# Performance work log

Hardware: AMD Instinct MI355X
Metric: run time of the kernel (lower is better)

## Reference

```python
import jax, jax.numpy as jnp
import numpy as np
import math

NH, NKV, HD = 8, 1, 128
SOFTCAP = 30.0
ROPE_BASE = 500000.0


def _rope_tables(T, hd, base):
    half = hd // 2
    inv_freq = 1.0 / (base ** (np.arange(half, dtype=np.float32) / half))
    t = np.arange(T, dtype=np.float32)
    ang = np.outer(t, inv_freq)  # [T, half]
    return jnp.asarray(np.cos(ang)), jnp.asarray(np.sin(ang))


def apply_rope(x, cos, sin):
    # x: [B, T, H, hd]; cos/sin: [T, hd//2]
    half = x.shape[-1] // 2
    x1, x2 = x[..., :half], x[..., half:]
    T = x.shape[1]
    c = cos[:T][None, :, None, :]
    s = sin[:T][None, :, None, :]
    return jnp.concatenate([x1 * c - x2 * s, x1 * s + x2 * c], axis=-1)


def setup_inputs() -> dict:
    key = jax.random.key(0)
    ks = jax.random.split(key, 5)
    B, T, D = 4, 2048, 1024
    KD = NKV * HD
    x = jax.random.normal(ks[0], (B, T, D), dtype=jnp.float32)
    Wq = jax.random.normal(ks[1], (D, D), dtype=jnp.float32) * (D ** -0.5)
    Wk = jax.random.normal(ks[2], (KD, D), dtype=jnp.float32) * (D ** -0.5)
    Wv = jax.random.normal(ks[3], (KD, D), dtype=jnp.float32) * (D ** -0.5)
    Wo = jax.random.normal(ks[4], (D, D), dtype=jnp.float32) * (D ** -0.5)
    qk_gain = jnp.full((NH,), 1.5, dtype=jnp.float32)  # qk_gain_init
    cos, sin = _rope_tables(T, HD, ROPE_BASE)
    return {"x": x, "Wq": Wq, "Wk": Wk, "Wv": Wv, "Wo": Wo,
            "qk_gain": qk_gain, "cos": cos, "sin": sin}


def reference(x, Wq, Wk, Wv, Wo, qk_gain, cos, sin):
    B, T, D = x.shape
    # projections (QuantLinear with qat disabled == plain linear, no bias)
    q = (x @ Wq.T).reshape(B, T, NH, HD)
    k = (x @ Wk.T).reshape(B, T, NKV, HD)
    v = (x @ Wv.T).reshape(B, T, NKV, HD)
    q = apply_rope(q, cos, sin)
    k = apply_rope(k, cos, sin)
    # learned per-head QK gain applied to queries
    q = q * qk_gain[None, None, :, 1 - 1][..., None] if False else q * qk_gain[None, None, :, None]
    # GQA: broadcast the single kv head across NH query heads
    scale = 1.0 / math.sqrt(HD)
    scores = jnp.einsum('bqhd,bkgd->bhqk', q, k) * scale  # g==NKV==1 broadcast
    # logit softcap before masking/softmax
    scores = SOFTCAP * jnp.tanh(scores / SOFTCAP)
    causal = jnp.tril(jnp.ones((T, T), dtype=bool))
    scores = jnp.where(causal[None, None], scores, -jnp.inf)
    attn = jax.nn.softmax(scores, axis=-1)  # [B, NH, T, T]
    out = jnp.einsum('bhqk,bkgd->bqhd', attn, v).reshape(B, T, NH * HD)
    return out @ Wo.T
```

## Files before the change

### kernel.cpp

```cpp
#include <hip/hip_runtime.h>
#include <hip/hip_bf16.h>

#define B_ 4
#define T_ 2048
#define D_ 1024
#define NH_ 8
#define HD_ 128

typedef short short8 __attribute__((ext_vector_type(8)));
typedef float floatx4 __attribute__((ext_vector_type(4)));
typedef float floatx16 __attribute__((ext_vector_type(16)));

#if __has_builtin(__builtin_amdgcn_exp2f)
#define EXP2F __builtin_amdgcn_exp2f
#else
#define EXP2F exp2f
#endif
#if __has_builtin(__builtin_amdgcn_rcpf)
#define RCPF __builtin_amdgcn_rcpf
#else
__device__ __forceinline__ float RCPF(float x) { return 1.f / x; }
#endif

#if __has_builtin(__builtin_amdgcn_global_load_lds)
#define G2L(gp, lp)                                                        \
  __builtin_amdgcn_global_load_lds(                                        \
      (const __attribute__((address_space(1))) unsigned int*)(gp),         \
      (__attribute__((address_space(3))) unsigned int*)(lp), 16, 0, 0)
#else
#define G2L(gp, lp) (*(uint4*)(lp) = *(const uint4*)(gp))
#endif

__device__ __forceinline__ unsigned short f2b(float f) {
  union { float fl; unsigned int i; } v; v.fl = f;
  unsigned int r = v.i + 0x7fffu + ((v.i >> 16) & 1u);
  return (unsigned short)(r >> 16);
}
__device__ __forceinline__ unsigned int pack_bf16(float a, float b) {
  unsigned int ua = __float_as_uint(a) + 0x8000u;
  unsigned int ub = __float_as_uint(b) + 0x8000u;
  return (ua >> 16) | (ub & 0xffff0000u);
}
__device__ __forceinline__ float blo(unsigned int u) { return __uint_as_float(u << 16); }
__device__ __forceinline__ float bhi(unsigned int u) { return __uint_as_float(u & 0xffff0000u); }

__global__ __launch_bounds__(256) void cvt_kernel(
    const float* __restrict__ x,  const float* __restrict__ wq,
    const float* __restrict__ wk, const float* __restrict__ wv,
    const float* __restrict__ wo, unsigned short* __restrict__ dst)
{
  size_t i = ((size_t)blockIdx.x * 256 + threadIdx.x) * 8;
  const float* src; size_t off;
  if      (i <  8388608u) { src = x;  off = i; }
  else if (i <  9437184u) { src = wq; off = i - 8388608u; }
  else if (i <  9568256u) { src = wk; off = i - 9437184u; }
  else if (i <  9699328u) { src = wv; off = i - 9568256u; }
  else                    { src = wo; off = i - 9699328u; }
  float4 a = *(const float4*)(src + off);
  float4 b = *(const float4*)(src + off + 4);
  uint4 o;
  o.x = pack_bf16(a.x, a.y); o.y = pack_bf16(a.z, a.w);
  o.z = pack_bf16(b.x, b.y); o.w = pack_bf16(b.z, b.w);
  *(uint4*)(dst + i) = o;
}

template <bool C_F32>
__device__ __forceinline__ void gemm_body_1024(
    const unsigned short* __restrict__ Arow0,
    const unsigned short* __restrict__ Btile,
    void* __restrict__ Cb, int ldC)
{
  __shared__ unsigned short As[128 * 32];
  __shared__ unsigned short Bs[128 * 32];
  const int tid = threadIdx.x;
  const int lane = tid & 63;
  const int w = tid >> 6;
  const int wr = w >> 1, wc = w & 1;
  const int l15 = lane & 15, quad = lane >> 4;

  const unsigned short* a_src = Arow0 + (size_t)(tid >> 2) * 1024 + (tid & 3) * 8;
  const unsigned short* b_src = Btile + (size_t)(tid >> 2) * 1024 + (tid & 3) * 8;
  unsigned short* a_dst = &As[(tid >> 2) * 32 + (tid & 3) * 8];
  unsigned short* b_dst = &Bs[(tid >> 2) * 32 + (tid & 3) * 8];

  floatx4 zero = {0.f, 0.f, 0.f, 0.f};
  floatx4 acc[4][4];
#pragma unroll
  for (int i = 0; i < 4; i++)
#pragma unroll
    for (int j = 0; j < 4; j++) acc[i][j] = zero;

  for (int k0 = 0; k0 < 1024; k0 += 32) {
    __syncthreads();
    G2L(a_src + k0,         a_dst);
    G2L(a_src + 65536 + k0, a_dst + 2048);
    G2L(b_src + k0,         b_dst);
    G2L(b_src + 65536 + k0, b_dst + 2048);
    __syncthreads();
    short8 af[4], bfr[4];
#pragma unroll
    for (int i = 0; i < 4; i++)
      af[i] = *(const short8*)&As[(wr * 64 + i * 16 + l15) * 32 + quad * 8];
#pragma unroll
    for (int j = 0; j < 4; j++)
      bfr[j] = *(const short8*)&Bs[(wc * 64 + j * 16 + l15) * 32 + quad * 8];
#pragma unroll
    for (int i = 0; i < 4; i++)
#pragma unroll
      for (int j = 0; j < 4; j++)
        acc[i][j] = __builtin_amdgcn_mfma_f32_16x16x32_bf16(af[i], bfr[j], acc[i][j], 0, 0, 0);
  }
#pragma unroll
  for (int i = 0; i < 4; i++)
#pragma unroll
    for (int j = 0; j < 4; j++)
#pragma unroll
      for (int r = 0; r < 4; r++) {
        size_t off = (size_t)(wr * 64 + i * 16 + quad * 4 + r) * ldC + wc * 64 + j * 16 + l15;
        if (C_F32) ((float*)Cb)[off] = acc[i][j][r];
        else ((unsigned short*)Cb)[off] = f2b(acc[i][j][r]);
      }
}

__global__ __launch_bounds__(256) void gemm_qkv_kernel(
    const unsigned short* __restrict__ x,
    const unsigned short* __restrict__ Wq,
    const unsigned short* __restrict__ Wk,
    const unsigned short* __restrict__ Wv,
    unsigned short* __restrict__ q,
    unsigned short* __restrict__ k,
    unsigned short* __restrict__ v)
{
  const int bx = blockIdx.x, by = blockIdx.y;
  const unsigned short* Btile;
  unsigned short* C;
  int ldC, col0;
  if (by < 8) { Btile = Wq + (size_t)by * 128 * 1024; C = q; ldC = 1024; col0 = by * 128; }
  else if (by == 8) { Btile = Wk; C = k; ldC = 128; col0 = 0; }
  else { Btile = Wv; C = v; ldC = 128; col0 = 0; }
  gemm_body_1024<false>(x + (size_t)bx * 128 * 1024, Btile,
                        C + (size_t)bx * 128 * ldC + col0, ldC);
}

__global__ __launch_bounds__(256) void gemm_out_kernel(
    const unsigned short* __restrict__ ao,
    const unsigned short* __restrict__ Wo,
    float* __restrict__ out)
{
  const int bx = blockIdx.x, by = blockIdx.y;
  gemm_body_1024<true>(ao + (size_t)bx * 128 * 1024, Wo + (size_t)by * 128 * 1024,
                       out + (size_t)bx * 128 * 1024 + by * 128, 1024);
}

__global__ __launch_bounds__(256) void prep_kernel(
    unsigned short* __restrict__ q,
    unsigned short* __restrict__ k,
    const unsigned short* __restrict__ v,
    unsigned short* __restrict__ vT,
    const float* __restrict__ cosT,
    const float* __restrict__ sinT,
    const float* __restrict__ gain)
{
  __shared__ unsigned short tile[32 * 136];
  const int tid = threadIdx.x;
  if (blockIdx.x < 256) {
    const int b = blockIdx.x >> 6, t0 = (blockIdx.x & 63) * 32;
    for (int u = tid; u < 512; u += 256) {
      int r = u >> 4, c = u & 15;
      *(uint4*)&tile[r * 136 + c * 8] =
          *(const uint4*)(v + ((size_t)(b * T_ + t0 + r)) * 128 + c * 8);
    }
    __syncthreads();
    for (int u = tid; u < 512; u += 256) {
      int d = u >> 2, c = u & 3;
      short8 val;
#pragma unroll
      for (int j = 0; j < 8; j++) val[j] = (short)tile[(c * 8 + j) * 136 + d];
      *(short8*)(vT + ((size_t)(b * 128 + d)) * T_ + t0 + c * 8) = val;
    }
    return;
  }
  int idx = (blockIdx.x - 256) * 256 + tid;
  unsigned short* ptr;
  size_t base;
  int t, j;
  float g;
  if (idx < 524288) {
    j = idx & 7;
    int h = (idx >> 3) & 7;
    int bt = idx >> 6;
    t = bt & (T_ - 1);
    base = (size_t)bt * 1024 + h * 128 + j * 8;
    ptr = q;
    g = gain[h] * 0.0029462782549439484f;
  } else {
    int id = idx - 524288;
    j = id & 7;
    int bt = id >> 3;
    t = bt & (T_ - 1);
    base = (size_t)bt * 128 + j * 8;
    ptr = k;
    g = 1.f;
  }
  float4 ca = *(const float4*)&cosT[t * 64 + j * 8];
  float4 cb = *(const float4*)&cosT[t * 64 + j * 8 + 4];
  float4 sa = *(const float4*)&sinT[t * 64 + j * 8];
  float4 sb = *(const float4*)&sinT[t * 64 + j * 8 + 4];
  uint4 lo = *(const uint4*)(ptr + base);
  uint4 hi = *(const uint4*)(ptr + base + 64);
  uint4 olo, ohi;
  {
    float a0 = blo(lo.x), a1 = bhi(lo.x), b0 = blo(hi.x), b1 = bhi(hi.x);
    olo.x = pack_bf16((a0 * ca.x - b0 * sa.x) * g, (a1 * ca.y - b1 * sa.y) * g);
    ohi.x = pack_bf16((a0 * sa.x + b0 * ca.x) * g, (a1 * sa.y + b1 * ca.y) * g);
  }
  {
    float a0 = blo(lo.y), a1 = bhi(lo.y), b0 = blo(hi.y), b1 = bhi(hi.y);
    olo.y = pack_bf16((a0 * ca.z - b0 * sa.z) * g, (a1 * ca.w - b1 * sa.w) * g);
    ohi.y = pack_bf16((a0 * sa.z + b0 * ca.z) * g, (a1 * sa.w + b1 * ca.w) * g);
  }
  {
    float a0 = blo(lo.z), a1 = bhi(lo.z), b0 = blo(hi.z), b1 = bhi(hi.z);
    olo.z = pack_bf16((a0 * cb.x - b0 * sb.x) * g, (a1 * cb.y - b1 * sb.y) * g);
    ohi.z = pack_bf16((a0 * sb.x + b0 * cb.x) * g, (a1 * sb.y + b1 * cb.y) * g);
  }
  {
    float a0 = blo(lo.w), a1 = bhi(lo.w), b0 = blo(hi.w), b1 = bhi(hi.w);
    olo.w = pack_bf16((a0 * cb.z - b0 * sb.z) * g, (a1 * cb.w - b1 * sb.w) * g);
    ohi.w = pack_bf16((a0 * sb.z + b0 * cb.z) * g, (a1 * sb.w + b1 * cb.w) * g);
  }
  *(uint4*)(ptr + base) = olo;
  *(uint4*)(ptr + base + 64) = ohi;
}

template <int NSPLIT>
__global__ __launch_bounds__(256, 3) void attn_kernel(
    const unsigned short* __restrict__ q,
    const unsigned short* __restrict__ k,
    const unsigned short* __restrict__ vT,
    unsigned short* __restrict__ ao,
    unsigned short* __restrict__ Opart,
    float* __restrict__ lbuf)
{
  __shared__ unsigned short Ks[2][16 * 264];
  __shared__ unsigned short Vts[2][128 * 40];

  const int h = blockIdx.y, b = blockIdx.z;
  const int pr   = blockIdx.x / NSPLIT;
  const int part = blockIdx.x % NSPLIT;
  const int tid = threadIdx.x, lane = tid & 63, w = tid >> 6;
  const int q32 = lane & 31, hi = lane >> 5;

  const unsigned short* ksrc =
      k + (size_t)b * T_ * 128 + (size_t)(tid >> 4) * 128 + (tid & 15) * 8;
  const int koff0 = (tid & 15) * 264 + (tid >> 4) * 8;
  const int koff1 = koff0 + 16 * 8;
  const unsigned short* vsrc =
      vT + (size_t)b * 128 * T_ + (size_t)(tid >> 2) * T_ + (tid & 3) * 8;
  const int voff0 = (tid >> 2) * 40 + (tid & 3) * 8;
  const int voff1 = voff0 + 64 * 40;

  for (int pass = 0; pass < 2; pass++) {
    const int qblock = pass ? (15 - pr) : pr;
    const int qw = qblock * 128 + w * 32;
    const int nkt = 4 * qblock + 4;
    const int base = nkt / NSPLIT, rem = nkt % NSPLIT;
    const int ktBeg = part * base + (part < rem ? part : rem);
    const int ktEnd = ktBeg + base + (part < rem ? 1 : 0);

    short8 qf[8];
    {
      const unsigned short* qrow =
          q + ((size_t)(b * T_ + qw + q32) * NH_ + h) * HD_ + hi * 8;
#pragma unroll
      for (int c = 0; c < 8; c++) qf[c] = *(const short8*)(qrow + c * 16);
    }

    float l_i = 0.f;
    floatx16 acc[4];
#pragma unroll
    for (int dt = 0; dt < 4; dt++)
#pragma unroll
      for (int r = 0; r < 16; r++) acc[dt][r] = 0.f;

    __syncthreads();
    {
      uint4 kr0 = *(const uint4*)(ksrc + (size_t)ktBeg * 4096);
      uint4 kr1 = *(const uint4*)(ksrc + (size_t)ktBeg * 4096 + 2048);
      uint4 vr0 = *(const uint4*)(vsrc + ktBeg * 32);
      uint4 vr1 = *(const uint4*)(vsrc + (size_t)64 * T_ + ktBeg * 32);
      unsigned short* kb = Ks[ktBeg & 1];
      unsigned short* vb = Vts[ktBeg & 1];
      *(uint4*)(kb + koff0) = kr0; *(uint4*)(kb + koff1) = kr1;
      *(uint4*)(vb + voff0) = vr0; *(uint4*)(vb + voff1) = vr1;
    }

    for (int kt = ktBeg; kt < ktEnd; kt++) {
      __syncthreads();
      uint4 kr0, kr1, vr0, vr1;
      const bool more = (kt + 1 < ktEnd);
      if (more) {
        kr0 = *(const uint4*)(ksrc + (size_t)(kt + 1) * 4096);
        kr1 = *(const uint4*)(ksrc + (size_t)(kt + 1) * 4096 + 2048);
        vr0 = *(const uint4*)(vsrc + (kt + 1) * 32);
        vr1 = *(const uint4*)(vsrc + (size_t)64 * T_ + (kt + 1) * 32);
      }

      if (kt * 32 <= qw + 31) {
        const unsigned short* KsC = Ks[kt & 1];
        const unsigned short* VtC = Vts[kt & 1];
        floatx16 st;
#pragma unroll
        for (int r = 0; r < 16; r++) st[r] = 0.f;
#pragma unroll
        for (int c = 0; c < 8; c++) {
          short8 kf = *(const short8*)&KsC[(2 * c + hi) * 264 + q32 * 8];
          st = __builtin_amdgcn_mfma_f32_32x32x16_bf16(kf, qf[c], st, 0, 0, 0);
        }
        float rs = 0.f;
        unsigned int A[8];
        if (kt * 32 + 31 <= qw) {
          float pv[16];
#pragma unroll
          for (int r = 0; r < 16; r++) {
            float s = st[r];
            float e = EXP2F(2.8853901f * s);
            float u = RCPF(e + 1.f);
            float p = EXP2F(-86.561707f * u);
            pv[r] = p;
            rs += p;
          }
#pragma unroll
          for (int m = 0; m < 8; m++) A[m] = pack_bf16(pv[2 * m], pv[2 * m + 1]);
        } else {
          const int qrow = qw + q32;
          float pv[16];
#pragma unroll
          for (int r = 0; r < 16; r++) {
            float s = st[r];
            float e = EXP2F(2.8853901f * s);
            float u = RCPF(e + 1.f);
            float p = EXP2F(-86.561707f * u);
            int key = kt * 32 + (r & 3) + 8 * (r >> 2) + 4 * hi;
            p = (key <= qrow) ? p : 0.f;
            pv[r] = p;
            rs += p;
          }
#pragma unroll
          for (int m = 0; m < 8; m++) A[m] = pack_bf16(pv[2 * m], pv[2 * m + 1]);
        }
        unsigned int a0 = A[0], a1 = A[1], a2 = A[2], a3 = A[3];
        unsigned int a4 = A[4], a5 = A[5], a6 = A[6], a7 = A[7];
        asm("v_permlane32_swap_b32 %0, %1" : "+v"(a0), "+v"(a2));
        asm("v_permlane32_swap_b32 %0, %1" : "+v"(a1), "+v"(a3));
        asm("v_permlane32_swap_b32 %0, %1" : "+v"(a4), "+v"(a6));
        asm("v_permlane32_swap_b32 %0, %1" : "+v"(a5), "+v"(a7));
        uint4 u0; u0.x = a0; u0.y = a1; u0.z = a2; u0.w = a3;
        uint4 u1; u1.x = a4; u1.y = a5; u1.z = a6; u1.w = a7;
        short8 pf0 = *(short8*)&u0;
        short8 pf1 = *(short8*)&u1;
        l_i += rs + __shfl_xor(rs, 32);
#pragma unroll
        for (int dt = 0; dt < 4; dt++) {
          short8 v0 = *(const short8*)&VtC[(dt * 32 + q32) * 40 + hi * 8];
          short8 v1 = *(const short8*)&VtC[(dt * 32 + q32) * 40 + 16 + hi * 8];
          acc[dt] = __builtin_amdgcn_mfma_f32_32x32x16_bf16(v0, pf0, acc[dt], 0, 0, 0);
          acc[dt] = __builtin_amdgcn_mfma_f32_32x32x16_bf16(v1, pf1, acc[dt], 0, 0, 0);
        }
      }

      if (more) {
        unsigned short* kb = Ks[(kt + 1) & 1];
        unsigned short* vb = Vts[(kt + 1) & 1];
        *(uint4*)(kb + koff0) = kr0; *(uint4*)(kb + koff1) = kr1;
        *(uint4*)(vb + voff0) = vr0; *(uint4*)(vb + voff1) = vr1;
      }
    }

    {
      const size_t rowidx = (size_t)(b * T_ + qw + q32) * NH_ + h;
      if (NSPLIT == 1) {
        float linv = 1.f / l_i;
        unsigned short* aop = ao + rowidx * HD_;
#pragma unroll
        for (int dt = 0; dt < 4; dt++)
#pragma unroll
          for (int rg = 0; rg < 4; rg++) {
            uint2 o;
            o.x = pack_bf16(acc[dt][4 * rg + 0] * linv, acc[dt][4 * rg + 1] * linv);
            o.y = pack_bf16(acc[dt][4 * rg + 2] * linv, acc[dt][4 * rg + 3] * linv);
            *(uint2*)(aop + dt * 32 + rg * 8 + hi * 4) = o;
          }
      } else {
        unsigned short* dst =
            ((part == NSPLIT - 1) ? ao : Opart + (size_t)part * 8388608u) +
            rowidx * HD_;
#pragma unroll
        for (int dt = 0; dt < 4; dt++)
#pragma unroll
          for (int rg = 0; rg < 4; rg++) {
            uint2 o;
            o.x = pack_bf16(acc[dt][4 * rg + 0], acc[dt][4 * rg + 1]);
            o.y = pack_bf16(acc[dt][4 * rg + 2], acc[dt][4 * rg + 3]);
            *(uint2*)(dst + dt * 32 + rg * 8 + hi * 4) = o;
          }
        if (hi == 0) lbuf[(size_t)part * 65536u + rowidx] = l_i;
      }
    }
  }
}

template <int NSPLIT>
__global__ __launch_bounds__(256) void combine_kernel(
    const unsigned short* __restrict__ Opart,
    const float* __restrict__ lbuf,
    unsigned short* __restrict__ ao)
{
  size_t i = ((size_t)blockIdx.x * 256 + threadIdx.x) * 8;
  size_t r = i >> 7;
  float ls = 0.f;
#pragma unroll
  for (int p = 0; p < NSPLIT; p++) ls += lbuf[(size_t)p * 65536u + r];
  float linv = RCPF(ls);
  uint4 c = *(const uint4*)(ao + i);
  float v0 = blo(c.x), v1 = bhi(c.x), v2 = blo(c.y), v3 = bhi(c.y);
  float v4 = blo(c.z), v5 = bhi(c.z), v6 = blo(c.w), v7 = bhi(c.w);
#pragma unroll
  for (int p = 0; p < NSPLIT - 1; p++) {
    uint4 a = *(const uint4*)(Opart + (size_t)p * 8388608u + i);
    v0 += blo(a.x); v1 += bhi(a.x); v2 += blo(a.y); v3 += bhi(a.y);
    v4 += blo(a.z); v5 += bhi(a.z); v6 += blo(a.w); v7 += bhi(a.w);
  }
  uint4 o;
  o.x = pack_bf16(v0 * linv, v1 * linv);
  o.y = pack_bf16(v2 * linv, v3 * linv);
  o.z = pack_bf16(v4 * linv, v5 * linv);
  o.w = pack_bf16(v6 * linv, v7 * linv);
  *(uint4*)(ao + i) = o;
}

extern "C" void kernel_launch(void* const* d_in, const int* in_sizes, int n_in,
                              void* d_out, int out_size, void* d_ws, size_t ws_size,
                              hipStream_t stream) {
  const float* x    = (const float*)d_in[0];
  const float* Wq   = (const float*)d_in[1];
  const float* Wk   = (const float*)d_in[2];
  const float* Wv   = (const float*)d_in[3];
  const float* Wo   = (const float*)d_in[4];
  const float* gain = (const float*)d_in[5];
  const float* cosT = (const float*)d_in[6];
  const float* sinT = (const float*)d_in[7];
  float* out = (float*)d_out;

  unsigned short* ws = (unsigned short*)d_ws;
  unsigned short* blob = ws;
  unsigned short* xb  = blob;
  unsigned short* Wqb = blob + 8388608u;
  unsigned short* Wkb = blob + 9437184u;
  unsigned short* Wvb = blob + 9568256u;
  unsigned short* Wob = blob + 9699328u;
  unsigned short* q   = ws + 10747904u;
  unsigned short* kk  = ws + 19136512u;
  unsigned short* v   = ws + 20185088u;
  unsigned short* vT  = ws + 21233664u;
  unsigned short* ao  = xb;
  unsigned short* Opart = ws + 22282240u;
  float* l2 = (float*)((char*)d_ws + 61341696u);
  const size_t need2 = 61865984ull;
  float* l3 = (float*)((char*)d_ws + 78118912u);
  const size_t need3 = 78905344ull;

  cvt_kernel<<<5248, 256, 0, stream>>>(x, Wq, Wk, Wv, Wo, blob);
  gemm_qkv_kernel<<<dim3(64, 10), 256, 0, stream>>>(xb, Wqb, Wkb, Wvb, q, kk, v);
  prep_kernel<<<2560, 256, 0, stream>>>(q, kk, v, vT, cosT, sinT, gain);
  if (ws_size >= need3) {
    attn_kernel<3><<<dim3(24, 8, 4), 256, 0, stream>>>(q, kk, vT, ao, Opart, l3);
    combine_kernel<3><<<4096, 256, 0, stream>>>(Opart, l3, ao);
  } else if (ws_size >= need2) {
    attn_kernel<2><<<dim3(16, 8, 4), 256, 0, stream>>>(q, kk, vT, ao, Opart, l2);
    combine_kernel<2><<<4096, 256, 0, stream>>>(Opart, l2, ao);
  } else {
    attn_kernel<1><<<dim3(8, 8, 4), 256, 0, stream>>>(q, kk, vT, ao, Opart, l2);
  }
  gemm_out_kernel<<<dim3(64, 8), 256, 0, stream>>>(ao, Wob, out);
}
```

Measured before the change: 234.0 us.

## Fuse RoPE and QK gain into QKV GEMM epilogue; split QK accumulators, add setprio

Moves the RoPE rotation and the per-head gain scaling of Q and K into the QKV GEMM epilogue. The B-fragment column mapping is rearranged so each wave holds both halves (d and d+64) of a head dimension pair. This removes the separate elementwise prep pass that read and rewrote q and k, so prep now only transposes V. In attention, the QK^T MFMA chain is split into two independent accumulators to shorten the dependency chain, and the MFMA sections are wrapped in s_setprio to favour matrix issue. The epilogue now does scattered fp32 cos/sin loads, and the B-fragment change may cause LDS bank conflicts.

```diff
diff --git a/kernel.cpp b/kernel.cpp
--- a/kernel.cpp
+++ b/kernel.cpp
@@ -64,11 +64,13 @@
   *(uint4*)(dst + i) = o;
 }
 
-template <bool C_F32>
+template <int MODE>
 __device__ __forceinline__ void gemm_body_1024(
     const unsigned short* __restrict__ Arow0,
     const unsigned short* __restrict__ Btile,
-    void* __restrict__ Cb, int ldC)
+    void* __restrict__ Cb, int ldC,
+    const float* __restrict__ cosT, const float* __restrict__ sinT,
+    float g, int tq0)
 {
   __shared__ unsigned short As[128 * 32];
   __shared__ unsigned short Bs[128 * 32];
@@ -102,24 +104,47 @@
     for (int i = 0; i < 4; i++)
       af[i] = *(const short8*)&As[(wr * 64 + i * 16 + l15) * 32 + quad * 8];
 #pragma unroll
-    for (int j = 0; j < 4; j++)
-      bfr[j] = *(const short8*)&Bs[(wc * 64 + j * 16 + l15) * 32 + quad * 8];
+    for (int j = 0; j < 4; j++) {
+      const int cb = (MODE == 2) ? ((j < 2) ? wc * 32 + j * 16
+                                            : 64 + wc * 32 + (j - 2) * 16)
+                                 : wc * 64 + j * 16;
+      bfr[j] = *(const short8*)&Bs[(cb + l15) * 32 + quad * 8];
+    }
 #pragma unroll
     for (int i = 0; i < 4; i++)
 #pragma unroll
       for (int j = 0; j < 4; j++)
         acc[i][j] = __builtin_amdgcn_mfma_f32_16x16x32_bf16(af[i], bfr[j], acc[i][j], 0, 0, 0);
   }
-#pragma unroll
-  for (int i = 0; i < 4; i++)
-#pragma unroll
-    for (int j = 0; j < 4; j++)
-#pragma unroll
-      for (int r = 0; r < 4; r++) {
-        size_t off = (size_t)(wr * 64 + i * 16 + quad * 4 + r) * ldC + wc * 64 + j * 16 + l15;
-        if (C_F32) ((float*)Cb)[off] = acc[i][j][r];
-        else ((unsigned short*)Cb)[off] = f2b(acc[i][j][r]);
-      }
+  if (MODE == 2) {
+#pragma unroll
+    for (int i = 0; i < 4; i++)
+#pragma unroll
+      for (int j = 0; j < 2; j++)
+#pragma unroll
+        for (int r = 0; r < 4; r++) {
+          const int row = wr * 64 + i * 16 + quad * 4 + r;
+          const int tm = tq0 + row;
+          const int d = wc * 32 + j * 16 + l15;
+          float cv = cosT[tm * 64 + d];
+          float sv = sinT[tm * 64 + d];
+          float a = acc[i][j][r], b2 = acc[i][j + 2][r];
+          unsigned short* cp = (unsigned short*)Cb + (size_t)row * ldC + d;
+          cp[0]  = f2b((a * cv - b2 * sv) * g);
+          cp[64] = f2b((a * sv + b2 * cv) * g);
+        }
+  } else {
+#pragma unroll
+    for (int i = 0; i < 4; i++)
+#pragma unroll
+      for (int j = 0; j < 4; j++)
+#pragma unroll
+        for (int r = 0; r < 4; r++) {
+          size_t off = (size_t)(wr * 64 + i * 16 + quad * 4 + r) * ldC + wc * 64 + j * 16 + l15;
+          if (MODE == 1) ((float*)Cb)[off] = acc[i][j][r];
+          else ((unsigned short*)Cb)[off] = f2b(acc[i][j][r]);
+        }
+  }
 }
 
 __global__ __launch_bounds__(256) void gemm_qkv_kernel(
@@ -129,17 +154,26 @@
     const unsigned short* __restrict__ Wv,
     unsigned short* __restrict__ q,
     unsigned short* __restrict__ k,
-    unsigned short* __restrict__ v)
+    unsigned short* __restrict__ v,
+    const float* __restrict__ gain,
+    const float* __restrict__ cosT,
+    const float* __restrict__ sinT)
 {
   const int bx = blockIdx.x, by = blockIdx.y;
-  const unsigned short* Btile;
-  unsigned short* C;
-  int ldC, col0;
-  if (by < 8) { Btile = Wq + (size_t)by * 128 * 1024; C = q; ldC = 1024; col0 = by * 128; }
-  else if (by == 8) { Btile = Wk; C = k; ldC = 128; col0 = 0; }
-  else { Btile = Wv; C = v; ldC = 128; col0 = 0; }
-  gemm_body_1024<false>(x + (size_t)bx * 128 * 1024, Btile,
-                        C + (size_t)bx * 128 * ldC + col0, ldC);
+  const unsigned short* A = x + (size_t)bx * 128 * 1024;
+  const int tq0 = (bx & 15) * 128;
+  if (by < 8) {
+    float g = gain[by] * 0.0029462782549439484f;
+    gemm_body_1024<2>(A, Wq + (size_t)by * 128 * 1024,
+                      q + (size_t)bx * 128 * 1024 + by * 128, 1024,
+                      cosT, sinT, g, tq0);
+  } else if (by == 8) {
+    gemm_body_1024<2>(A, Wk, k + (size_t)bx * 128 * 128, 128,
+                      cosT, sinT, 1.f, tq0);
+  } else {
+    gemm_body_1024<0>(A, Wv, v + (size_t)bx * 128 * 128, 128,
+                      nullptr, nullptr, 1.f, 0);
+  }
 }
 
 __global__ __launch_bounds__(256) void gemm_out_kernel(
@@ -148,89 +182,31 @@
     float* __restrict__ out)
 {
   const int bx = blockIdx.x, by = blockIdx.y;
-  gemm_body_1024<true>(ao + (size_t)bx * 128 * 1024, Wo + (size_t)by * 128 * 1024,
-                       out + (size_t)bx * 128 * 1024 + by * 128, 1024);
+  gemm_body_1024<1>(ao + (size_t)bx * 128 * 1024, Wo + (size_t)by * 128 * 1024,
+                    out + (size_t)bx * 128 * 1024 + by * 128, 1024,
+                    nullptr, nullptr, 1.f, 0);
 }
 
 __global__ __launch_bounds__(256) void prep_kernel(
-    unsigned short* __restrict__ q,
-    unsigned short* __restrict__ k,
     const unsigned short* __restrict__ v,
-    unsigned short* __restrict__ vT,
-    const float* __restrict__ cosT,
-    const float* __restrict__ sinT,
-    const float* __restrict__ gain)
+    unsigned short* __restrict__ vT)
 {
   __shared__ unsigned short tile[32 * 136];
   const int tid = threadIdx.x;
-  if (blockIdx.x < 256) {
-    const int b = blockIdx.x >> 6, t0 = (blockIdx.x & 63) * 32;
-    for (int u = tid; u < 512; u += 256) {
-      int r = u >> 4, c = u & 15;
-      *(uint4*)&tile[r * 136 + c * 8] =
-          *(const uint4*)(v + ((size_t)(b * T_ + t0 + r)) * 128 + c * 8);
-    }
-    __syncthreads();
-    for (int u = tid; u < 512; u += 256) {
-      int d = u >> 2, c = u & 3;
-      short8 val;
-#pragma unroll
-      for (int j = 0; j < 8; j++) val[j] = (short)tile[(c * 8 + j) * 136 + d];
-      *(short8*)(vT + ((size_t)(b * 128 + d)) * T_ + t0 + c * 8) = val;
-    }
-    return;
-  }
-  int idx = (blockIdx.x - 256) * 256 + tid;
-  unsigned short* ptr;
-  size_t base;
-  int t, j;
-  float g;
-  if (idx < 524288) {
-    j = idx & 7;
-    int h = (idx >> 3) & 7;
-    int bt = idx >> 6;
-    t = bt & (T_ - 1);
-    base = (size_t)bt * 1024 + h * 128 + j * 8;
-    ptr = q;
-    g = gain[h] * 0.0029462782549439484f;
-  } else {
-    int id = idx - 524288;
-    j = id & 7;
-    int bt = id >> 3;
-    t = bt & (T_ - 1);
-    base = (size_t)bt * 128 + j * 8;
-    ptr = k;
-    g = 1.f;
-  }
-  float4 ca = *(const float4*)&cosT[t * 64 + j * 8];
-  float4 cb = *(const float4*)&cosT[t * 64 + j * 8 + 4];
-  float4 sa = *(const float4*)&sinT[t * 64 + j * 8];
-  float4 sb = *(const float4*)&sinT[t * 64 + j * 8 + 4];
-  uint4 lo = *(const uint4*)(ptr + base);
-  uint4 hi = *(const uint4*)(ptr + base + 64);
-  uint4 olo, ohi;
-  {
-    float a0 = blo(lo.x), a1 = bhi(lo.x), b0 = blo(hi.x), b1 = bhi(hi.x);
-    olo.x = pack_bf16((a0 * ca.x - b0 * sa.x) * g, (a1 * ca.y - b1 * sa.y) * g);
-    ohi.x = pack_bf16((a0 * sa.x + b0 * ca.x) * g, (a1 * sa.y + b1 * ca.y) * g);
-  }
-  {
-    float a0 = blo(lo.y), a1 = bhi(lo.y), b0 = blo(hi.y), b1 = bhi(hi.y);
-    olo.y = pack_bf16((a0 * ca.z - b0 * sa.z) * g, (a1 * ca.w - b1 * sa.w) * g);
-    ohi.y = pack_bf16((a0 * sa.z + b0 * ca.z) * g, (a1 * sa.w + b1 * ca.w) * g);
-  }
-  {
-    float a0 = blo(lo.z), a1 = bhi(lo.z), b0 = blo(hi.z), b1 = bhi(hi.z);
-    olo.z = pack_bf16((a0 * cb.x - b0 * sb.x) * g, (a1 * cb.y - b1 * sb.y) * g);
-    ohi.z = pack_bf16((a0 * sb.x + b0 * cb.x) * g, (a1 * sb.y + b1 * cb.y) * g);
-  }
-  {
-    float a0 = blo(lo.w), a1 = bhi(lo.w), b0 = blo(hi.w), b1 = bhi(hi.w);
-    olo.w = pack_bf16((a0 * cb.z - b0 * sb.z) * g, (a1 * cb.w - b1 * sb.w) * g);
-    ohi.w = pack_bf16((a0 * sb.z + b0 * cb.z) * g, (a1 * sb.w + b1 * cb.w) * g);
-  }
-  *(uint4*)(ptr + base) = olo;
-  *(uint4*)(ptr + base + 64) = ohi;
+  const int b = blockIdx.x >> 6, t0 = (blockIdx.x & 63) * 32;
+  for (int u = tid; u < 512; u += 256) {
+    int r = u >> 4, c = u & 15;
+    *(uint4*)&tile[r * 136 + c * 8] =
+        *(const uint4*)(v + ((size_t)(b * T_ + t0 + r)) * 128 + c * 8);
+  }
+  __syncthreads();
+  for (int u = tid; u < 512; u += 256) {
+    int d = u >> 2, c = u & 3;
+    short8 val;
+#pragma unroll
+    for (int j = 0; j < 8; j++) val[j] = (short)tile[(c * 8 + j) * 136 + d];
+    *(short8*)(vT + ((size_t)(b * 128 + d)) * T_ + t0 + c * 8) = val;
+  }
 }
 
 template <int NSPLIT>
@@ -309,21 +285,26 @@
       if (kt * 32 <= qw + 31) {
         const unsigned short* KsC = Ks[kt & 1];
         const unsigned short* VtC = Vts[kt & 1];
-        floatx16 st;
-#pragma unroll
-        for (int r = 0; r < 16; r++) st[r] = 0.f;
+        floatx16 stA, stB;
+#pragma unroll
+        for (int r = 0; r < 16; r++) { stA[r] = 0.f; stB[r] = 0.f; }
+        __builtin_amdgcn_s_setprio(1);
 #pragma unroll
         for (int c = 0; c < 8; c++) {
           short8 kf = *(const short8*)&KsC[(2 * c + hi) * 264 + q32 * 8];
-          st = __builtin_amdgcn_mfma_f32_32x32x16_bf16(kf, qf[c], st, 0, 0, 0);
+          if (c & 1)
+            stB = __builtin_amdgcn_mfma_f32_32x32x16_bf16(kf, qf[c], stB, 0, 0, 0);
+          else
+            stA = __builtin_amdgcn_mfma_f32_32x32x16_bf16(kf, qf[c], stA, 0, 0, 0);
         }
+        __builtin_amdgcn_s_setprio(0);
         float rs = 0.f;
         unsigned int A[8];
         if (kt * 32 + 31 <= qw) {
           float pv[16];
 #pragma unroll
           for (int r = 0; r < 16; r++) {
-            float s = st[r];
+            float s = stA[r] + stB[r];
             float e = EXP2F(2.8853901f * s);
             float u = RCPF(e + 1.f);
             float p = EXP2F(-86.561707f * u);
@@ -337,7 +318,7 @@
           float pv[16];
 #pragma unroll
           for (int r = 0; r < 16; r++) {
-            float s = st[r];
+            float s = stA[r] + stB[r];
             float e = EXP2F(2.8853901f * s);
             float u = RCPF(e + 1.f);
             float p = EXP2F(-86.561707f * u);
@@ -360,6 +341,7 @@
         short8 pf0 = *(short8*)&u0;
         short8 pf1 = *(short8*)&u1;
         l_i += rs + __shfl_xor(rs, 32);
+        __builtin_amdgcn_s_setprio(1);
 #pragma unroll
         for (int dt = 0; dt < 4; dt++) {
           short8 v0 = *(const short8*)&VtC[(dt * 32 + q32) * 40 + hi * 8];
@@ -367,6 +349,7 @@
           acc[dt] = __builtin_amdgcn_mfma_f32_32x32x16_bf16(v0, pf0, acc[dt], 0, 0, 0);
           acc[dt] = __builtin_amdgcn_mfma_f32_32x32x16_bf16(v1, pf1, acc[dt], 0, 0, 0);
         }
+        __builtin_amdgcn_s_setprio(0);
       }
 
       if (more) {
@@ -471,8 +454,9 @@
   const size_t need3 = 78905344ull;
 
   cvt_kernel<<<5248, 256, 0, stream>>>(x, Wq, Wk, Wv, Wo, blob);
-  gemm_qkv_kernel<<<dim3(64, 10), 256, 0, stream>>>(xb, Wqb, Wkb, Wvb, q, kk, v);
-  prep_kernel<<<2560, 256, 0, stream>>>(q, kk, v, vT, cosT, sinT, gain);
+  gemm_qkv_kernel<<<dim3(64, 10), 256, 0, stream>>>(xb, Wqb, Wkb, Wvb, q, kk, v,
+                                                    gain, cosT, sinT);
+  prep_kernel<<<256, 256, 0, stream>>>(v, vT);
   if (ws_size >= need3) {
     attn_kernel<3><<<dim3(24, 8, 4), 256, 0, stream>>>(q, kk, vT, ao, Opart, l3);
     combine_kernel<3><<<4096, 256, 0, stream>>>(Opart, l3, ao);
```

Result: slower. 247.3 us (+5.7%).
